# Performance work log

Hardware: AMD Instinct MI355X
Metric: run time of the kernel (lower is better)

## Reference

```python
import jax, jax.numpy as jnp
import numpy as np

EPS = 1e-12
NEG = -1e30


def setup_inputs() -> dict:
    key = jax.random.key(0)
    ks = jax.random.split(key, 7)
    B, Nq, Lp, H, D = 96, 35, 180, 768, 128
    q_hidden = jax.random.normal(ks[0], (B, Nq, H), dtype=jnp.float32)
    pos_hidden = jax.random.normal(ks[1], (B, Lp, H), dtype=jnp.float32)
    neg_hidden = jax.random.normal(ks[2], (B, Lp, H), dtype=jnp.float32)
    W = jax.random.normal(ks[3], (H, D), dtype=jnp.float32) * 0.02
    b = jax.random.normal(ks[4], (D,), dtype=jnp.float32) * 0.02
    # non-punctuation filter mask; guarantee at least one valid token per passage
    pos_mask = jax.random.bernoulli(ks[5], 0.85, (B, Lp)).at[:, 0].set(True)
    neg_mask = jax.random.bernoulli(ks[6], 0.85, (B, Lp)).at[:, 0].set(True)
    return {"q_hidden": q_hidden, "pos_hidden": pos_hidden, "neg_hidden": neg_hidden,
            "W": W, "b": b, "pos_mask": pos_mask, "neg_mask": neg_mask}


def _vector_representation(h, W, b):
    # Linear projection then F.normalize(x) with torch default dim=1,
    # i.e. normalization over the SEQUENCE axis (faithful to source).
    x = jnp.einsum('blh,hd->bld', h, W) + b
    norm = jnp.maximum(jnp.sqrt(jnp.sum(x * x, axis=1, keepdims=True)), EPS)
    return x / norm


def _late_interaction(q, p, mask):
    # q: [Bq, Nq, D], p: [Bp, Lp, D], mask: [Bp, Lp] (True = keep token)
    sim = jnp.einsum('qnd,pld->qpnl', q, p)          # [Bq, Bp, Nq, Lp]
    sim = jnp.where(mask[None, :, None, :], sim, NEG)
    return jnp.max(sim, axis=-1).sum(axis=-1)        # MaxSim: max over Lp, sum over Nq


def reference(q_hidden, pos_hidden, neg_hidden, W, b, pos_mask, neg_mask):
    q = _vector_representation(q_hidden, W, b)
    pos = _vector_representation(pos_hidden, W, b)
    neg = _vector_representation(neg_hidden, W, b)
    pos_scores = _late_interaction(q, pos, pos_mask)
    neg_scores = _late_interaction(q, neg, neg_mask)
    return jnp.concatenate((pos_scores, neg_scores), axis=1)  # [B, 2B]
```

## Files before the change

### kernel.cpp

```cpp
#include <hip/hip_runtime.h>

typedef __attribute__((ext_vector_type(4))) float f32x4;
typedef __attribute__((ext_vector_type(8))) short s16x8;
typedef __attribute__((ext_vector_type(4))) short s16x4;
typedef __bf16 bf16x4 __attribute__((ext_vector_type(4)));

#define B_   96
#define NQ   35
#define LP   180
#define H_   768
#define D_   128
#define NEGF (-1e30f)

#define NROWS 37920
#define QROWS 3360
#define PROWS 17280

__device__ __forceinline__ unsigned short f2bf(float f) {
    return __builtin_bit_cast(unsigned short, (__bf16)f);
}

__device__ __forceinline__ s16x8 pack_bf16(f32x4 v0, f32x4 v1) {
    bf16x4 h0 = __builtin_convertvector(v0, bf16x4);
    bf16x4 h1 = __builtin_convertvector(v1, bf16x4);
    s16x4 a = __builtin_bit_cast(s16x4, h0), b = __builtin_bit_cast(s16x4, h1);
    return __builtin_shufflevector(a, b, 0, 1, 2, 3, 4, 5, 6, 7);
}

__device__ __forceinline__ void glds16(const void* g, void* l) {
    __builtin_amdgcn_global_load_lds(
        (const __attribute__((address_space(1))) unsigned int*)g,
        (__attribute__((address_space(3))) unsigned int*)l,
        16, 0, 0);
}

__global__ __launch_bounds__(256) void prep_k(
    const float* __restrict__ W, unsigned short* __restrict__ wthi,
    const void* __restrict__ pm, const void* __restrict__ nm,
    unsigned char* __restrict__ maskc) {
    __shared__ unsigned int rr[256];
    int b = blockIdx.x, t = threadIdx.x;
    if (b < 48) {
        int tid = b * 256 + t;
        int nt = tid / (24 * 64);
        int r = tid - nt * 24 * 64;
        int ks = r / 64, lane = r - ks * 64;
        int m = lane & 15, quad = lane >> 4;
        unsigned short* o = wthi + (size_t)tid * 8;
#pragma unroll
        for (int j = 0; j < 8; j++) {
            int k = ks * 32 + quad * 8 + j;
            o[j] = f2bf(W[(size_t)k * D_ + nt * 16 + m]);
        }
    } else {
        const unsigned int* pw = (const unsigned int*)pm;
        unsigned int f1 = 0, f3 = 0, f4 = 0;
        for (int w = t; w < 4320; w += 256) {
            unsigned int v = pw[w];
            f1 |= v & 0x0000ff00u;
            f3 |= v & 0xff000000u;
            if (w & 1) f4 |= v & 0x000000ffu;
        }
        rr[t] = f1; __syncthreads();
        for (int s2 = 128; s2; s2 >>= 1) { if (t < s2) rr[t] |= rr[t + s2]; __syncthreads(); }
        unsigned int c1 = rr[0]; __syncthreads();
        rr[t] = f3; __syncthreads();
        for (int s2 = 128; s2; s2 >>= 1) { if (t < s2) rr[t] |= rr[t + s2]; __syncthreads(); }
        unsigned int c3 = rr[0]; __syncthreads();
        rr[t] = f4; __syncthreads();
        for (int s2 = 128; s2; s2 >>= 1) { if (t < s2) rr[t] |= rr[t + s2]; __syncthreads(); }
        unsigned int c4 = rr[0];
        int i = (b - 48) * 256 + t;
        const void* src = (i < B_ * LP) ? pm : nm;
        int j = (i < B_ * LP) ? i : i - B_ * LP;
        bool bit;
        if (c1 > 0)       bit = ((const unsigned char*)src)[j] != 0;
        else if (c3 > 0)  bit = ((const float*)src)[j] != 0.0f;
        else if (c4 > 0)  bit = ((const int*)src)[j] != 0;
        else              bit = ((const long long*)src)[j] != 0;
        maskc[i] = bit ? 1 : 0;
    }
}

__global__ __launch_bounds__(512, 1) void proj_k(
    const float* __restrict__ qh, const float* __restrict__ ph, const float* __restrict__ nh,
    const unsigned short* __restrict__ wthi, const float* __restrict__ bias,
    const unsigned char* __restrict__ maskc,
    unsigned short* __restrict__ qfrag, unsigned short* __restrict__ pfrag) {
    __shared__ float sb[24576];
    int b = blockIdx.x, t = threadIdx.x;
    int wave = t >> 6, lane = t & 63;
    int m = lane & 15, quad = lane >> 4;
    unsigned short* xb = (unsigned short*)sb;

    if (b < 192) {
        const float* src = (b < 96) ? ph + (size_t)b * LP * H_
                                    : nh + (size_t)(b - 96) * LP * H_;
        const float* gp[6];
#pragma unroll
        for (int g = 0; g < 6; g++) {
            int rl = wave * 24 + g * 4 + (lane >> 4);
            int rc = rl < LP ? rl : LP - 1;
            gp[g] = src + (size_t)rc * H_ + (((lane & 15) ^ (2 * (rl & 7))) << 2);
        }

        f32x4 acc[12];
#pragma unroll
        for (int mt = 0; mt < 12; mt++) acc[mt] = (f32x4){0.f, 0.f, 0.f, 0.f};

        {
            float* d0 = sb + wave * 1536;
#pragma unroll
            for (int g = 0; g < 6; g++) glds16(gp[g], d0 + g * 256);
        }
        __syncthreads();

        for (int s = 0; s < 12; s++) {
            if (s < 11) {
                float* d0 = sb + ((s + 1) & 1) * 12288 + wave * 1536;
#pragma unroll
                for (int g = 0; g < 6; g++) glds16(gp[g] + (s + 1) * 64, d0 + g * 256);
            }
            const float* bb = sb + (s & 1) * 12288;
#pragma unroll
            for (int ksg = 0; ksg < 2; ksg++) {
                s16x8 bf = *(const s16x8*)(wthi +
                           ((size_t)(wave * 24 + s * 2 + ksg) * 64 + lane) * 8);
                int kc = ksg * 8 + quad * 2;
#pragma unroll
                for (int mt = 0; mt < 12; mt++) {
                    int row = mt * 16 + m;
                    const float* fb = bb + row * 64 + ((kc ^ (2 * (row & 7))) << 2);
                    f32x4 lo = *(const f32x4*)fb, hi = *(const f32x4*)(fb + 4);
                    acc[mt] = __builtin_amdgcn_mfma_f32_16x16x32_bf16(
                        pack_bf16(lo, hi), bf, acc[mt], 0, 0, 0);
                }
            }
            __syncthreads();
        }

        float bv = bias[wave * 16 + m];
        float s2 = 0.f;
#pragma unroll
        for (int mt = 0; mt < 12; mt++)
#pragma unroll
            for (int r = 0; r < 4; r++) {
                int prow = mt * 16 + quad * 4 + r;
                float v = acc[mt][r] + bv;
                acc[mt][r] = v;
                if (prow < LP) s2 += v * v;
            }
        s2 += __shfl_xor(s2, 16); s2 += __shfl_xor(s2, 32);
        float sc = rsqrtf(fmaxf(s2, 1e-24f));
        __syncthreads();
#pragma unroll
        for (int mt = 0; mt < 12; mt++)
#pragma unroll
            for (int r = 0; r < 4; r++) {
                int prow = mt * 16 + quad * 4 + r;
                if (prow < LP) xb[prow * 136 + wave * 16 + m] = f2bf(acc[mt][r] * sc);
            }
        __syncthreads();
        const unsigned char* mk = maskc + b * LP;
        unsigned short* pdst = pfrag + (size_t)b * 24576;
#pragma unroll
        for (int i = 0; i < 6; i++) {
            int ch = t + i * 512;
            int ln = ch & 63;
            int l = ((ch >> 8) << 4) + (ln & 15);
            int lsrc = (l < LP && mk[l]) ? l : 0;
            int d0 = ((ch >> 6) & 3) * 32 + (ln >> 4) * 8;
            *(s16x8*)&pdst[(size_t)ch * 8] = *(const s16x8*)&xb[lsrc * 136 + d0];
        }
    } else {
        int qp = b - 192;
        const float* src = qh + (size_t)qp * 70 * H_;
        const float* gp[3];
#pragma unroll
        for (int g = 0; g < 3; g++) {
            int rl = wave * 12 + g * 4 + (lane >> 4);
            int rc = rl < 70 ? rl : 69;
            gp[g] = src + (size_t)rc * H_ + (((lane & 15) ^ (2 * (rl & 7))) << 2);
        }

        f32x4 acc[5];
#pragma unroll
        for (int mt = 0; mt < 5; mt++) acc[mt] = (f32x4){0.f, 0.f, 0.f, 0.f};

        {
            float* d0 = sb + wave * 768;
#pragma unroll
            for (int g = 0; g < 3; g++) glds16(gp[g], d0 + g * 256);
        }
        __syncthreads();

        for (int s = 0; s < 12; s++) {
            if (s < 11) {
                float* d0 = sb + ((s + 1) & 1) * 6144 + wave * 768;
#pragma unroll
                for (int g = 0; g < 3; g++) glds16(gp[g] + (s + 1) * 64, d0 + g * 256);
            }
            const float* bb = sb + (s & 1) * 6144;
#pragma unroll
            for (int ksg = 0; ksg < 2; ksg++) {
                s16x8 bf = *(const s16x8*)(wthi +
                           ((size_t)(wave * 24 + s * 2 + ksg) * 64 + lane) * 8);
                int kc = ksg * 8 + quad * 2;
#pragma unroll
                for (int mt = 0; mt < 5; mt++) {
                    int row = mt * 16 + m;
                    const float* fb = bb + row * 64 + ((kc ^ (2 * (row & 7))) << 2);
                    f32x4 lo = *(const f32x4*)fb, hi = *(const f32x4*)(fb + 4);
                    acc[mt] = __builtin_amdgcn_mfma_f32_16x16x32_bf16(
                        pack_bf16(lo, hi), bf, acc[mt], 0, 0, 0);
                }
            }
            __syncthreads();
        }

        float bv = bias[wave * 16 + m];
        float s0 = 0.f, s1 = 0.f;
#pragma unroll
        for (int mt = 0; mt < 5; mt++)
#pragma unroll
            for (int r = 0; r < 4; r++) {
                int prow = mt * 16 + quad * 4 + r;
                float v = acc[mt][r] + bv;
                acc[mt][r] = v;
                if (prow < 35) s0 += v * v;
                else if (prow < 70) s1 += v * v;
            }
        s0 += __shfl_xor(s0, 16); s0 += __shfl_xor(s0, 32);
        s1 += __shfl_xor(s1, 16); s1 += __shfl_xor(s1, 32);
        float sc0 = rsqrtf(fmaxf(s0, 1e-24f));
        float sc1 = rsqrtf(fmaxf(s1, 1e-24f));
        __syncthreads();
#pragma unroll
        for (int mt = 0; mt < 5; mt++)
#pragma unroll
            for (int r = 0; r < 4; r++) {
                int prow = mt * 16 + quad * 4 + r;
                if (prow < 70)
                    xb[prow * 136 + wave * 16 + m] =
                        f2bf(acc[mt][r] * (prow < 35 ? sc0 : sc1));
            }
        __syncthreads();
        unsigned short* qdst = qfrag + (size_t)qp * 10240;
#pragma unroll
        for (int i = 0; i < 3; i++) {
            int ch = t + i * 512;
            if (ch < 1280) {
                int ln = ch & 63;
                int prow = ((ch >> 8) << 4) + (ln & 15);
                int d0 = ((ch >> 6) & 3) * 32 + (ln >> 4) * 8;
                s16x8 v = (s16x8){0, 0, 0, 0, 0, 0, 0, 0};
                if (prow < 70) v = *(const s16x8*)&xb[prow * 136 + d0];
                *(s16x8*)&qdst[(size_t)ch * 8] = v;
            }
        }
    }
}

__global__ __launch_bounds__(512, 1) void interact_k(
    const unsigned short* __restrict__ qfrag, const unsigned short* __restrict__ pfrag,
    float* __restrict__ out) {
    __shared__ unsigned short plds[24576];
    __shared__ float comb[2][4][2];
    int wave = threadIdx.x >> 6, lane = threadIdx.x & 63;
    int b = blockIdx.x;
    int xcd = b & 7, i = b >> 3;
    int c = xcd * 24 + (i % 24);
    int qgg = i / 24;
    int side = c / 96, pb = c - side * 96;
    int wq = wave & 3, half = wave >> 2;
    int m = lane & 15, quad = lane >> 4;

    const unsigned short* pbase = pfrag + (size_t)c * 24576;

#pragma unroll
    for (int g = 0; g < 2; g++) {
        int nt = wave + g * 8;
        if (nt < 12) {
#pragma unroll
            for (int ks = 0; ks < 4; ks++)
                glds16(pbase + ((size_t)(nt * 4 + ks) * 64 + lane) * 8,
                       &plds[(size_t)(nt * 4 + ks) * 512]);
        }
    }
    __syncthreads();

    const f32x4 zero4 = (f32x4){0.f, 0.f, 0.f, 0.f};

#pragma unroll 1
    for (int pass = 0; pass < 3; pass++) {
        int qp = (qgg * 3 + pass) * 4 + wq;
        const unsigned short* qbase = qfrag + (size_t)qp * 10240;
        float s0 = 0.f, s1 = 0.f;

        if (half == 0) {
            s16x8 a[3][4];
#pragma unroll
            for (int mt = 0; mt < 3; mt++)
#pragma unroll
                for (int ks = 0; ks < 4; ks++)
                    a[mt][ks] = *(const s16x8*)(qbase +
                                ((size_t)(mt * 4 + ks) * 64 + lane) * 8);
            float rmax[3][4];
#pragma unroll
            for (int mt = 0; mt < 3; mt++)
#pragma unroll
                for (int rr = 0; rr < 4; rr++) rmax[mt][rr] = NEGF;

            for (int nt = 0; nt < 12; nt++) {
                s16x8 bfr[4];
#pragma unroll
                for (int ks = 0; ks < 4; ks++)
                    bfr[ks] = *(const s16x8*)&plds[((size_t)(nt * 4 + ks) * 64 + lane) * 8];
                __builtin_amdgcn_s_setprio(1);
#pragma unroll
                for (int mt = 0; mt < 3; mt++) {
                    f32x4 acc = __builtin_amdgcn_mfma_f32_16x16x32_bf16(a[mt][0], bfr[0], zero4, 0, 0, 0);
                    acc = __builtin_amdgcn_mfma_f32_16x16x32_bf16(a[mt][1], bfr[1], acc, 0, 0, 0);
                    acc = __builtin_amdgcn_mfma_f32_16x16x32_bf16(a[mt][2], bfr[2], acc, 0, 0, 0);
                    acc = __builtin_amdgcn_mfma_f32_16x16x32_bf16(a[mt][3], bfr[3], acc, 0, 0, 0);
#pragma unroll
                    for (int rr = 0; rr < 4; rr++)
                        rmax[mt][rr] = fmaxf(rmax[mt][rr], acc[rr]);
                }
                __builtin_amdgcn_s_setprio(0);
            }
#pragma unroll
            for (int mt = 0; mt < 3; mt++)
#pragma unroll
                for (int rr = 0; rr < 4; rr++) {
                    float v = rmax[mt][rr];
                    v = fmaxf(v, __shfl_xor(v, 1));
                    v = fmaxf(v, __shfl_xor(v, 2));
                    v = fmaxf(v, __shfl_xor(v, 4));
                    v = fmaxf(v, __shfl_xor(v, 8));
                    int prow = mt * 16 + quad * 4 + rr;
                    if (prow < 35) s0 += v;
                    else if (prow < 70) s1 += v;
                }
        } else {
            s16x8 a[2][4];
#pragma unroll
            for (int mt = 0; mt < 2; mt++)
#pragma unroll
                for (int ks = 0; ks < 4; ks++)
                    a[mt][ks] = *(const s16x8*)(qbase +
                                ((size_t)((mt + 3) * 4 + ks) * 64 + lane) * 8);
            float rmax[2][4];
#pragma unroll
            for (int mt = 0; mt < 2; mt++)
#pragma unroll
                for (int rr = 0; rr < 4; rr++) rmax[mt][rr] = NEGF;

            for (int nt = 0; nt < 12; nt++) {
                s16x8 bfr[4];
#pragma unroll
                for (int ks = 0; ks < 4; ks++)
                    bfr[ks] = *(const s16x8*)&plds[((size_t)(nt * 4 + ks) * 64 + lane) * 8];
                __builtin_amdgcn_s_setprio(1);
#pragma unroll
                for (int mt = 0; mt < 2; mt++) {
                    f32x4 acc = __builtin_amdgcn_mfma_f32_16x16x32_bf16(a[mt][0], bfr[0], zero4, 0, 0, 0);
                    acc = __builtin_amdgcn_mfma_f32_16x16x32_bf16(a[mt][1], bfr[1], acc, 0, 0, 0);
                    acc = __builtin_amdgcn_mfma_f32_16x16x32_bf16(a[mt][2], bfr[2], acc, 0, 0, 0);
                    acc = __builtin_amdgcn_mfma_f32_16x16x32_bf16(a[mt][3], bfr[3], acc, 0, 0, 0);
#pragma unroll
                    for (int rr = 0; rr < 4; rr++)
                        rmax[mt][rr] = fmaxf(rmax[mt][rr], acc[rr]);
                }
                __builtin_amdgcn_s_setprio(0);
            }
#pragma unroll
            for (int mt = 0; mt < 2; mt++)
#pragma unroll
                for (int rr = 0; rr < 4; rr++) {
                    float v = rmax[mt][rr];
                    v = fmaxf(v, __shfl_xor(v, 1));
                    v = fmaxf(v, __shfl_xor(v, 2));
                    v = fmaxf(v, __shfl_xor(v, 4));
                    v = fmaxf(v, __shfl_xor(v, 8));
                    int prow = (mt + 3) * 16 + quad * 4 + rr;
                    if (prow < 35) s0 += v;
                    else if (prow < 70) s1 += v;
                }
        }

        s0 += __shfl_xor(s0, 16); s0 += __shfl_xor(s0, 32);
        s1 += __shfl_xor(s1, 16); s1 += __shfl_xor(s1, 32);
        if (lane == 0) { comb[half][wq][0] = s0; comb[half][wq][1] = s1; }
        __syncthreads();
        if (half == 0 && lane == 0) {
            int qb0 = qp * 2, qb1 = qp * 2 + 1;
            out[(size_t)qb0 * (2 * B_) + side * B_ + pb] = s0 + comb[1][wq][0];
            out[(size_t)qb1 * (2 * B_) + side * B_ + pb] = s1 + comb[1][wq][1];
        }
        __syncthreads();
    }
}

extern "C" void kernel_launch(void* const* d_in, const int* in_sizes, int n_in,
                              void* d_out, int out_size, void* d_ws, size_t ws_size,
                              hipStream_t stream) {
    const float* qh   = (const float*)d_in[0];
    const float* ph   = (const float*)d_in[1];
    const float* nh   = (const float*)d_in[2];
    const float* W    = (const float*)d_in[3];
    const float* bias = (const float*)d_in[4];
    const void* pmask = d_in[5];
    const void* nmask = d_in[6];
    float* out = (float*)d_out;
    char* ws = (char*)d_ws;

    constexpr size_t WTHI_OFF  = 256;
    constexpr size_t MASKC_OFF = WTHI_OFF + 196608;
    constexpr size_t QFRAG_OFF = MASKC_OFF + 34560;
    constexpr size_t PFRAG_OFF = QFRAG_OFF + 983040;

    unsigned short* wthi   = (unsigned short*)(ws + WTHI_OFF);
    unsigned char* maskc   = (unsigned char*)(ws + MASKC_OFF);
    unsigned short* qfrag  = (unsigned short*)(ws + QFRAG_OFF);
    unsigned short* pfrag  = (unsigned short*)(ws + PFRAG_OFF);

    prep_k<<<183, 256, 0, stream>>>(W, wthi, pmask, nmask, maskc);
    proj_k<<<240, 512, 0, stream>>>(qh, ph, nh, wthi, bias, maskc, qfrag, pfrag);
    interact_k<<<768, 512, 0, stream>>>(qfrag, pfrag, out);
}
```

Before: 188.4 us.

## Triple-buffer projection loads with explicit vmcnt waits and single barrier per stage

Replaces the double-buffered global-to-LDS pipeline in the projection kernel with a three-stage ring buffer, prefetching two stages ahead. Each iteration waits on the vector-memory counter for the oldest stage only, then issues one barrier instead of two syncthreads. The aim is to keep more loads in flight and cut barrier stalls, in exchange for a larger LDS footprint of 144KB. It also relies on vmcnt ordering assumptions that would break if the compiler placed other global loads in the loop, such as the wthi fragment loads.

```diff
diff --git a/kernel.cpp b/kernel.cpp
--- a/kernel.cpp
+++ b/kernel.cpp
@@ -33,6 +33,16 @@
         (__attribute__((address_space(3))) unsigned int*)l,
         16, 0, 0);
 }
+
+#define WAITV(N) do {                                                 \
+    asm volatile("s_waitcnt vmcnt(" #N ")" ::: "memory");             \
+    __builtin_amdgcn_sched_barrier(0);                                \
+} while (0)
+
+#define BAR() do {                                                    \
+    __builtin_amdgcn_sched_barrier(0);                                \
+    __builtin_amdgcn_s_barrier();                                     \
+} while (0)
 
 __global__ __launch_bounds__(256) void prep_k(
     const float* __restrict__ W, unsigned short* __restrict__ wthi,
@@ -87,12 +97,24 @@
     const unsigned short* __restrict__ wthi, const float* __restrict__ bias,
     const unsigned char* __restrict__ maskc,
     unsigned short* __restrict__ qfrag, unsigned short* __restrict__ pfrag) {
-    __shared__ float sb[24576];
+    __shared__ float sb[36864];
     int b = blockIdx.x, t = threadIdx.x;
     int wave = t >> 6, lane = t & 63;
     int m = lane & 15, quad = lane >> 4;
     unsigned short* xb = (unsigned short*)sb;
 
+#define PSTAGE(S) do {                                                \
+    float* d0 = sb + ((S) % 3) * 12288 + wave * 1536;                 \
+    _Pragma("unroll")                                                 \
+    for (int g = 0; g < 6; g++) glds16(gp[g] + (S) * 64, d0 + g * 256); \
+} while (0)
+
+#define QSTAGE(S) do {                                                \
+    float* d0 = sb + ((S) % 3) * 6144 + wave * 768;                   \
+    _Pragma("unroll")                                                 \
+    for (int g = 0; g < 3; g++) glds16(gp[g] + (S) * 64, d0 + g * 256); \
+} while (0)
+
     if (b < 192) {
         const float* src = (b < 96) ? ph + (size_t)b * LP * H_
                                     : nh + (size_t)(b - 96) * LP * H_;
@@ -108,20 +130,14 @@
 #pragma unroll
         for (int mt = 0; mt < 12; mt++) acc[mt] = (f32x4){0.f, 0.f, 0.f, 0.f};
 
-        {
-            float* d0 = sb + wave * 1536;
-#pragma unroll
-            for (int g = 0; g < 6; g++) glds16(gp[g], d0 + g * 256);
-        }
-        __syncthreads();
+        PSTAGE(0);
+        PSTAGE(1);
 
         for (int s = 0; s < 12; s++) {
-            if (s < 11) {
-                float* d0 = sb + ((s + 1) & 1) * 12288 + wave * 1536;
-#pragma unroll
-                for (int g = 0; g < 6; g++) glds16(gp[g] + (s + 1) * 64, d0 + g * 256);
-            }
-            const float* bb = sb + (s & 1) * 12288;
+            if (s < 11) WAITV(6); else WAITV(0);
+            BAR();
+            if (s < 10) PSTAGE(s + 2);
+            const float* bb = sb + (s % 3) * 12288;
 #pragma unroll
             for (int ksg = 0; ksg < 2; ksg++) {
                 s16x8 bf = *(const s16x8*)(wthi +
@@ -136,7 +152,6 @@
                         pack_bf16(lo, hi), bf, acc[mt], 0, 0, 0);
                 }
             }
-            __syncthreads();
         }
 
         float bv = bias[wave * 16 + m];
@@ -187,20 +202,14 @@
 #pragma unroll
         for (int mt = 0; mt < 5; mt++) acc[mt] = (f32x4){0.f, 0.f, 0.f, 0.f};
 
-        {
-            float* d0 = sb + wave * 768;
-#pragma unroll
-            for (int g = 0; g < 3; g++) glds16(gp[g], d0 + g * 256);
-        }
-        __syncthreads();
+        QSTAGE(0);
+        QSTAGE(1);
 
         for (int s = 0; s < 12; s++) {
-            if (s < 11) {
-                float* d0 = sb + ((s + 1) & 1) * 6144 + wave * 768;
-#pragma unroll
-                for (int g = 0; g < 3; g++) glds16(gp[g] + (s + 1) * 64, d0 + g * 256);
-            }
-            const float* bb = sb + (s & 1) * 6144;
+            if (s < 11) WAITV(3); else WAITV(0);
+            BAR();
+            if (s < 10) QSTAGE(s + 2);
+            const float* bb = sb + (s % 3) * 6144;
 #pragma unroll
             for (int ksg = 0; ksg < 2; ksg++) {
                 s16x8 bf = *(const s16x8*)(wthi +
@@ -215,7 +224,6 @@
                         pack_bf16(lo, hi), bf, acc[mt], 0, 0, 0);
                 }
             }
-            __syncthreads();
         }
 
         float bv = bias[wave * 16 + m];
@@ -259,6 +267,8 @@
             }
         }
     }
+#undef PSTAGE
+#undef QSTAGE
 }
 
 __global__ __launch_bounds__(512, 1) void interact_k(
```

Result: no change. 191.2 us (+1.5%).

## Retile projection GEMM into 4x2 wave grid to cut LDS A-fragment reads

Applied to the files above, without the earlier changes.

The projection kernel changes the wave decomposition. Before, each wave owned a 16-column slice and walked all row tiles. Now each wave owns a 3x4 (or 2x4 for queries) block of 16x16 tiles across rows and columns, so each A fragment loaded from LDS and converted to bf16 feeds four MFMAs. The LDS swizzle changes from 2*(row&7) to row&15 to spread bank accesses. The per-column sequence-axis norm now needs a cross-wave reduction through shared memory, which adds an extra barrier, and each wave now holds four B fragments, which raises register pressure.

```diff
diff --git a/kernel.cpp b/kernel.cpp
--- a/kernel.cpp
+++ b/kernel.cpp
@@ -91,7 +91,9 @@
     int b = blockIdx.x, t = threadIdx.x;
     int wave = t >> 6, lane = t & 63;
     int m = lane & 15, quad = lane >> 4;
+    int mg = wave & 3, ng = wave >> 2;
     unsigned short* xb = (unsigned short*)sb;
+    float* ssql = sb + 23040;
 
     if (b < 192) {
         const float* src = (b < 96) ? ph + (size_t)b * LP * H_
@@ -101,12 +103,14 @@
         for (int g = 0; g < 6; g++) {
             int rl = wave * 24 + g * 4 + (lane >> 4);
             int rc = rl < LP ? rl : LP - 1;
-            gp[g] = src + (size_t)rc * H_ + (((lane & 15) ^ (2 * (rl & 7))) << 2);
-        }
-
-        f32x4 acc[12];
-#pragma unroll
-        for (int mt = 0; mt < 12; mt++) acc[mt] = (f32x4){0.f, 0.f, 0.f, 0.f};
+            gp[g] = src + (size_t)rc * H_ + (((lane & 15) ^ (rl & 15)) << 2);
+        }
+
+        f32x4 acc[3][4];
+#pragma unroll
+        for (int mtl = 0; mtl < 3; mtl++)
+#pragma unroll
+            for (int ntl = 0; ntl < 4; ntl++) acc[mtl][ntl] = (f32x4){0.f, 0.f, 0.f, 0.f};
 
         {
             float* d0 = sb + wave * 1536;
@@ -124,42 +128,76 @@
             const float* bb = sb + (s & 1) * 12288;
 #pragma unroll
             for (int ksg = 0; ksg < 2; ksg++) {
-                s16x8 bf = *(const s16x8*)(wthi +
-                           ((size_t)(wave * 24 + s * 2 + ksg) * 64 + lane) * 8);
+                s16x8 bf[4];
+#pragma unroll
+                for (int ntl = 0; ntl < 4; ntl++)
+                    bf[ntl] = *(const s16x8*)(wthi +
+                              ((size_t)((ng * 4 + ntl) * 24 + s * 2 + ksg) * 64 + lane) * 8);
                 int kc = ksg * 8 + quad * 2;
 #pragma unroll
-                for (int mt = 0; mt < 12; mt++) {
-                    int row = mt * 16 + m;
-                    const float* fb = bb + row * 64 + ((kc ^ (2 * (row & 7))) << 2);
-                    f32x4 lo = *(const f32x4*)fb, hi = *(const f32x4*)(fb + 4);
-                    acc[mt] = __builtin_amdgcn_mfma_f32_16x16x32_bf16(
-                        pack_bf16(lo, hi), bf, acc[mt], 0, 0, 0);
+                for (int mtl = 0; mtl < 3; mtl++) {
+                    int row = (mtl * 4 + mg) * 16 + m;
+                    int sw = row & 15;
+                    const float* rbase = bb + row * 64;
+                    f32x4 lo = *(const f32x4*)(rbase + ((kc ^ sw) << 2));
+                    f32x4 hi = *(const f32x4*)(rbase + (((kc + 1) ^ sw) << 2));
+                    s16x8 af = pack_bf16(lo, hi);
+#pragma unroll
+                    for (int ntl = 0; ntl < 4; ntl++)
+                        acc[mtl][ntl] = __builtin_amdgcn_mfma_f32_16x16x32_bf16(
+                            af, bf[ntl], acc[mtl][ntl], 0, 0, 0);
                 }
             }
             __syncthreads();
         }
 
-        float bv = bias[wave * 16 + m];
-        float s2 = 0.f;
-#pragma unroll
-        for (int mt = 0; mt < 12; mt++)
-#pragma unroll
-            for (int r = 0; r < 4; r++) {
-                int prow = mt * 16 + quad * 4 + r;
-                float v = acc[mt][r] + bv;
-                acc[mt][r] = v;
-                if (prow < LP) s2 += v * v;
-            }
-        s2 += __shfl_xor(s2, 16); s2 += __shfl_xor(s2, 32);
-        float sc = rsqrtf(fmaxf(s2, 1e-24f));
-        __syncthreads();
-#pragma unroll
-        for (int mt = 0; mt < 12; mt++)
-#pragma unroll
-            for (int r = 0; r < 4; r++) {
-                int prow = mt * 16 + quad * 4 + r;
-                if (prow < LP) xb[prow * 136 + wave * 16 + m] = f2bf(acc[mt][r] * sc);
-            }
+        float bvv[4], part[4];
+#pragma unroll
+        for (int ntl = 0; ntl < 4; ntl++) {
+            bvv[ntl] = bias[ng * 64 + ntl * 16 + m];
+            part[ntl] = 0.f;
+        }
+#pragma unroll
+        for (int mtl = 0; mtl < 3; mtl++)
+#pragma unroll
+            for (int ntl = 0; ntl < 4; ntl++)
+#pragma unroll
+                for (int r = 0; r < 4; r++) {
+                    int prow = (mtl * 4 + mg) * 16 + quad * 4 + r;
+                    float v = acc[mtl][ntl][r] + bvv[ntl];
+                    acc[mtl][ntl][r] = v;
+                    if (prow < LP) part[ntl] += v * v;
+                }
+#pragma unroll
+        for (int ntl = 0; ntl < 4; ntl++) {
+            part[ntl] += __shfl_xor(part[ntl], 16);
+            part[ntl] += __shfl_xor(part[ntl], 32);
+        }
+        if (quad == 0) {
+#pragma unroll
+            for (int ntl = 0; ntl < 4; ntl++)
+                ssql[mg * 128 + ng * 64 + ntl * 16 + m] = part[ntl];
+        }
+        __syncthreads();
+        float sc[4];
+#pragma unroll
+        for (int ntl = 0; ntl < 4; ntl++) {
+            int col = ng * 64 + ntl * 16 + m;
+            float s2 = ssql[col] + ssql[128 + col] + ssql[256 + col] + ssql[384 + col];
+            sc[ntl] = rsqrtf(fmaxf(s2, 1e-24f));
+        }
+        __syncthreads();
+#pragma unroll
+        for (int mtl = 0; mtl < 3; mtl++)
+#pragma unroll
+            for (int ntl = 0; ntl < 4; ntl++)
+#pragma unroll
+                for (int r = 0; r < 4; r++) {
+                    int prow = (mtl * 4 + mg) * 16 + quad * 4 + r;
+                    if (prow < LP)
+                        xb[prow * 136 + ng * 64 + ntl * 16 + m] =
+                            f2bf(acc[mtl][ntl][r] * sc[ntl]);
+                }
         __syncthreads();
         const unsigned char* mk = maskc + b * LP;
         unsigned short* pdst = pfrag + (size_t)b * 24576;
@@ -180,12 +218,14 @@
         for (int g = 0; g < 3; g++) {
             int rl = wave * 12 + g * 4 + (lane >> 4);
             int rc = rl < 70 ? rl : 69;
-            gp[g] = src + (size_t)rc * H_ + (((lane & 15) ^ (2 * (rl & 7))) << 2);
-        }
-
-        f32x4 acc[5];
-#pragma unroll
-        for (int mt = 0; mt < 5; mt++) acc[mt] = (f32x4){0.f, 0.f, 0.f, 0.f};
+            gp[g] = src + (size_t)rc * H_ + (((lane & 15) ^ (rl & 15)) << 2);
+        }
+
+        f32x4 acc[2][4];
+#pragma unroll
+        for (int mtl = 0; mtl < 2; mtl++)
+#pragma unroll
+            for (int ntl = 0; ntl < 4; ntl++) acc[mtl][ntl] = (f32x4){0.f, 0.f, 0.f, 0.f};
 
         {
             float* d0 = sb + wave * 768;
@@ -203,47 +243,97 @@
             const float* bb = sb + (s & 1) * 6144;
 #pragma unroll
             for (int ksg = 0; ksg < 2; ksg++) {
-                s16x8 bf = *(const s16x8*)(wthi +
-                           ((size_t)(wave * 24 + s * 2 + ksg) * 64 + lane) * 8);
+                s16x8 bf[4];
+#pragma unroll
+                for (int ntl = 0; ntl < 4; ntl++)
+                    bf[ntl] = *(const s16x8*)(wthi +
+                              ((size_t)((ng * 4 + ntl) * 24 + s * 2 + ksg) * 64 + lane) * 8);
                 int kc = ksg * 8 + quad * 2;
 #pragma unroll
-                for (int mt = 0; mt < 5; mt++) {
-                    int row = mt * 16 + m;
-                    const float* fb = bb + row * 64 + ((kc ^ (2 * (row & 7))) << 2);
-                    f32x4 lo = *(const f32x4*)fb, hi = *(const f32x4*)(fb + 4);
-                    acc[mt] = __builtin_amdgcn_mfma_f32_16x16x32_bf16(
-                        pack_bf16(lo, hi), bf, acc[mt], 0, 0, 0);
+                for (int mtl = 0; mtl < 2; mtl++) {
+                    int mi = mtl * 4 + mg;
+                    if (mi < 5) {
+                        int row = mi * 16 + m;
+                        int sw = row & 15;
+                        const float* rbase = bb + row * 64;
+                        f32x4 lo = *(const f32x4*)(rbase + ((kc ^ sw) << 2));
+                        f32x4 hi = *(const f32x4*)(rbase + (((kc + 1) ^ sw) << 2));
+                        s16x8 af = pack_bf16(lo, hi);
+#pragma unroll
+                        for (int ntl = 0; ntl < 4; ntl++)
+                            acc[mtl][ntl] = __builtin_amdgcn_mfma_f32_16x16x32_bf16(
+                                af, bf[ntl], acc[mtl][ntl], 0, 0, 0);
+                    }
                 }
             }
             __syncthreads();
         }
 
-        float bv = bias[wave * 16 + m];
-        float s0 = 0.f, s1 = 0.f;
-#pragma unroll
-        for (int mt = 0; mt < 5; mt++)
-#pragma unroll
-            for (int r = 0; r < 4; r++) {
-                int prow = mt * 16 + quad * 4 + r;
-                float v = acc[mt][r] + bv;
-                acc[mt][r] = v;
-                if (prow < 35) s0 += v * v;
-                else if (prow < 70) s1 += v * v;
-            }
-        s0 += __shfl_xor(s0, 16); s0 += __shfl_xor(s0, 32);
-        s1 += __shfl_xor(s1, 16); s1 += __shfl_xor(s1, 32);
-        float sc0 = rsqrtf(fmaxf(s0, 1e-24f));
-        float sc1 = rsqrtf(fmaxf(s1, 1e-24f));
-        __syncthreads();
-#pragma unroll
-        for (int mt = 0; mt < 5; mt++)
-#pragma unroll
-            for (int r = 0; r < 4; r++) {
-                int prow = mt * 16 + quad * 4 + r;
-                if (prow < 70)
-                    xb[prow * 136 + wave * 16 + m] =
-                        f2bf(acc[mt][r] * (prow < 35 ? sc0 : sc1));
-            }
+        float bvv[4], p0[4], p1[4];
+#pragma unroll
+        for (int ntl = 0; ntl < 4; ntl++) {
+            bvv[ntl] = bias[ng * 64 + ntl * 16 + m];
+            p0[ntl] = 0.f; p1[ntl] = 0.f;
+        }
+#pragma unroll
+        for (int mtl = 0; mtl < 2; mtl++) {
+            int mi = mtl * 4 + mg;
+            if (mi < 5) {
+#pragma unroll
+                for (int ntl = 0; ntl < 4; ntl++)
+#pragma unroll
+                    for (int r = 0; r < 4; r++) {
+                        int prow = mi * 16 + quad * 4 + r;
+                        float v = acc[mtl][ntl][r] + bvv[ntl];
+                        acc[mtl][ntl][r] = v;
+                        if (prow < 35) p0[ntl] += v * v;
+                        else if (prow < 70) p1[ntl] += v * v;
+                    }
+            }
+        }
+#pragma unroll
+        for (int ntl = 0; ntl < 4; ntl++) {
+            p0[ntl] += __shfl_xor(p0[ntl], 16); p0[ntl] += __shfl_xor(p0[ntl], 32);
+            p1[ntl] += __shfl_xor(p1[ntl], 16); p1[ntl] += __shfl_xor(p1[ntl], 32);
+        }
+        if (quad == 0) {
+#pragma unroll
+            for (int ntl = 0; ntl < 4; ntl++) {
+                int col = ng * 64 + ntl * 16 + m;
+                ssql[(mg * 128 + col) * 2 + 0] = p0[ntl];
+                ssql[(mg * 128 + col) * 2 + 1] = p1[ntl];
+            }
+        }
+        __syncthreads();
+        float sc0[4], sc1[4];
+#pragma unroll
+        for (int ntl = 0; ntl < 4; ntl++) {
+            int col = ng * 64 + ntl * 16 + m;
+            float a0 = 0.f, a1 = 0.f;
+#pragma unroll
+            for (int g2 = 0; g2 < 4; g2++) {
+                a0 += ssql[(g2 * 128 + col) * 2 + 0];
+                a1 += ssql[(g2 * 128 + col) * 2 + 1];
+            }
+            sc0[ntl] = rsqrtf(fmaxf(a0, 1e-24f));
+            sc1[ntl] = rsqrtf(fmaxf(a1, 1e-24f));
+        }
+        __syncthreads();
+#pragma unroll
+        for (int mtl = 0; mtl < 2; mtl++) {
+            int mi = mtl * 4 + mg;
+            if (mi < 5) {
+#pragma unroll
+                for (int ntl = 0; ntl < 4; ntl++)
+#pragma unroll
+                    for (int r = 0; r < 4; r++) {
+                        int prow = mi * 16 + quad * 4 + r;
+                        if (prow < 70)
+                            xb[prow * 136 + ng * 64 + ntl * 16 + m] =
+                                f2bf(acc[mtl][ntl][r] * (prow < 35 ? sc0[ntl] : sc1[ntl]));
+                    }
+            }
+        }
         __syncthreads();
         unsigned short* qdst = qfrag + (size_t)qp * 10240;
 #pragma unroll
```

New measurement: 187.7 us. No clear change (-0.3%).
